# Kernel tuning notes

Hardware: AMD Instinct MI355X
Metric: run time of the kernel (lower is better)

The kernel has to match this reference:

```python
import jax, jax.numpy as jnp
import numpy as np

B, IN, H, OUT, L = 16384, 256, 256, 256, 7  # L = hidden_lstm_layer (cells beyond input cell)


def setup_inputs() -> dict:
    key = jax.random.key(0)
    ks = jax.random.split(key, 13)
    s = 0.05
    return {
        "x": jax.random.normal(ks[0], (B, IN), jnp.float32),
        "h_all": jax.random.normal(ks[1], (L + 1, B, H), jnp.float32),
        "c_all": jax.random.normal(ks[2], (L + 1, B, H), jnp.float32),
        # input LSTMCell params
        "Wih0": jax.random.normal(ks[3], (4 * H, IN), jnp.float32) * s,
        "Whh0": jax.random.normal(ks[4], (4 * H, H), jnp.float32) * s,
        "bih0": jax.random.normal(ks[5], (4 * H,), jnp.float32) * s,
        "bhh0": jax.random.normal(ks[6], (4 * H,), jnp.float32) * s,
        # stacked hidden LSTMCell params
        "Wih": jax.random.normal(ks[7], (L, 4 * H, H), jnp.float32) * s,
        "Whh": jax.random.normal(ks[8], (L, 4 * H, H), jnp.float32) * s,
        "bih": jax.random.normal(ks[9], (L, 4 * H), jnp.float32) * s,
        "bhh": jax.random.normal(ks[10], (L, 4 * H), jnp.float32) * s,
        # output Linear
        "Wout": jax.random.normal(ks[11], (OUT, H), jnp.float32) * s,
        "bout": jax.random.normal(ks[12], (OUT,), jnp.float32) * s,
    }


def _lstm_cell(x, h, c, Wi, Wh, bi, bh):
    # PyTorch LSTMCell: gates in (i, f, g, o) order along the 4H axis
    gates = x @ Wi.T + h @ Wh.T + (bi + bh)  # [B, 4H]
    i, f, g, o = jnp.split(gates, 4, axis=-1)
    c_new = jax.nn.sigmoid(f) * c + jax.nn.sigmoid(i) * jnp.tanh(g)
    h_new = jax.nn.sigmoid(o) * jnp.tanh(c_new)
    return h_new, c_new


def reference(x, h_all, c_all, Wih0, Whh0, bih0, bhh0, Wih, Whh, bih, bhh, Wout, bout):
    h, c = _lstm_cell(x, h_all[0], c_all[0], Wih0, Whh0, bih0, bhh0)
    hs, cs = [h], [c]
    for l in range(L):  # sequential layer-to-layer recurrence (structural)
        h, c = _lstm_cell(h, h_all[l + 1], c_all[l + 1], Wih[l], Whh[l], bih[l], bhh[l])
        hs.append(h)
        cs.append(c)
    output = h @ Wout.T + bout  # [B, OUT]
    return output, jnp.stack(hs), jnp.stack(cs)
```

## Files before the change

kernel.cpp:

```cpp
#include <hip/hip_runtime.h>
#include <stdint.h>

typedef __bf16 bf16;
typedef bf16 bf16x8 __attribute__((ext_vector_type(8)));
typedef bf16 bf16x4 __attribute__((ext_vector_type(4)));
typedef float f32x4 __attribute__((ext_vector_type(4)));

#define BROWS 16384
#define BM 128
#define BK 64
#define SL ((size_t)BROWS * 256)

__device__ __forceinline__ float sigmoidf_(float x) { return 1.0f / (1.0f + __expf(-x)); }
__device__ __forceinline__ float tanhf_(float x)    { return 1.0f - 2.0f / (1.0f + __expf(2.0f * x)); }

__device__ __forceinline__ bf16x4 cvt4(float4 v) {
    bf16x4 b; b[0] = (bf16)v.x; b[1] = (bf16)v.y; b[2] = (bf16)v.z; b[3] = (bf16)v.w;
    return b;
}

__device__ __forceinline__ void gload_lds16(const void* g, void* l) {
    __builtin_amdgcn_global_load_lds(
        (const __attribute__((address_space(1))) void*)g,
        (__attribute__((address_space(3))) void*)l, 16, 0, 0);
}


__global__ void convert_all(
    const float* __restrict__ s0, bf16* __restrict__ d0, unsigned n0,
    const float* __restrict__ s1, bf16* __restrict__ d1, unsigned n1,
    const float* __restrict__ s2, bf16* __restrict__ d2, unsigned n2,
    const float* __restrict__ s3, bf16* __restrict__ d3, unsigned n3,
    const float* __restrict__ s4, bf16* __restrict__ d4, unsigned n4,
    const float* __restrict__ s5, bf16* __restrict__ d5, unsigned n5,
    const float* __restrict__ s6, bf16* __restrict__ d6, unsigned n6)
{
    const unsigned total = n0 + n1 + n2 + n3 + n4 + n5 + n6;
    const unsigned stride = gridDim.x * blockDim.x;
    for (unsigned i = blockIdx.x * blockDim.x + threadIdx.x; i < total; i += stride) {
        unsigned idx = i;
        const float* src; bf16* dst;
        if      (idx < n0)         { src = s0; dst = d0; }
        else if ((idx -= n0) < n1) { src = s1; dst = d1; }
        else if ((idx -= n1) < n2) { src = s2; dst = d2; }
        else if ((idx -= n2) < n3) { src = s3; dst = d3; }
        else if ((idx -= n3) < n4) { src = s4; dst = d4; }
        else if ((idx -= n4) < n5) { src = s5; dst = d5; }
        else                       { idx -= n5; src = s6; dst = d6; }
        float4 v = *(const float4*)(src + (size_t)idx * 4);
        *(bf16x4*)(dst + (size_t)idx * 4) = cvt4(v);
    }
}

__global__ __launch_bounds__(256, 4) void lstm_cell_bf16(
    const bf16* __restrict__ A1, const bf16* __restrict__ A2,
    const bf16* __restrict__ W1, const bf16* __restrict__ W2,
    const float* __restrict__ b1, const float* __restrict__ b2,
    const float* __restrict__ Cin,
    float* __restrict__ Hout, float* __restrict__ Cout,
    bf16* __restrict__ Hb)
{
    __shared__ __align__(16) bf16 As[BM * BK];
    __shared__ __align__(16) bf16 Bs[BM * BK];

    const int tid  = threadIdx.x;
    const int lane = tid & 63;
    const int wave = tid >> 6;
    const int wm   = wave >> 1;
    const int wn   = wave & 1;
    const int quad = lane >> 4;
    const int l15  = lane & 15;
    const int row0 = blockIdx.x * BM;
    const int jblk = blockIdx.y * 32;

    const int srow  = lane >> 3;
    const int sslot = lane & 7;

    size_t aOff[4], bOff[4]; int ldsOff[4];
#pragma unroll
    for (int r4 = 0; r4 < 4; ++r4) {
        int rowT = r4 * 32 + wave * 8 + srow;
        int gsl  = (sslot ^ (rowT & 7)) * 8;
        aOff[r4] = (size_t)(row0 + rowT) * 256 + gsl;
        int gate = (rowT >> 4) & 3;
        int j    = jblk + (rowT & 15) + ((rowT >> 6) << 4);
        bOff[r4] = (size_t)(gate * 256 + j) * 256 + gsl;
        ldsOff[r4] = (r4 * 32 + wave * 8) * BK;
    }

    f32x4 acc[4][4];
#pragma unroll
    for (int i = 0; i < 4; ++i)
#pragma unroll
        for (int jj = 0; jj < 4; ++jj)
#pragma unroll
            for (int r = 0; r < 4; ++r) acc[i][jj][r] = 0.0f;

    for (int kIter = 0; kIter < 8; ++kIter) {
        const bf16* aSrc; const bf16* wSrc; int k0;
        if (kIter < 4) { aSrc = A1; wSrc = W1; k0 = kIter * BK; }
        else           { aSrc = A2; wSrc = W2; k0 = (kIter - 4) * BK; }

        __syncthreads();
#pragma unroll
        for (int r4 = 0; r4 < 4; ++r4)
            gload_lds16(aSrc + aOff[r4] + k0, &As[ldsOff[r4]]);
#pragma unroll
        for (int r4 = 0; r4 < 4; ++r4)
            gload_lds16(wSrc + bOff[r4] + k0, &Bs[ldsOff[r4]]);
        __syncthreads();

#pragma unroll
        for (int kk = 0; kk < BK; kk += 32) {
            const int sl0 = (kk >> 3) + quad;
            bf16x8 af[4], bfr[4];
#pragma unroll
            for (int mi = 0; mi < 4; ++mi) {
                int row = wm * 64 + mi * 16 + l15;
                int ps  = sl0 ^ (row & 7);
                af[mi] = *(const bf16x8*)&As[row * BK + ps * 8];
            }
#pragma unroll
            for (int ni = 0; ni < 4; ++ni) {
                int row = wn * 64 + ni * 16 + l15;
                int ps  = sl0 ^ (row & 7);
                bfr[ni] = *(const bf16x8*)&Bs[row * BK + ps * 8];
            }
#pragma unroll
            for (int mi = 0; mi < 4; ++mi)
#pragma unroll
                for (int ni = 0; ni < 4; ++ni)
                    acc[mi][ni] = __builtin_amdgcn_mfma_f32_16x16x32_bf16(
                        af[mi], bfr[ni], acc[mi][ni], 0, 0, 0);
        }
    }

    const int j = jblk + wn * 16 + l15;
    float bsum[4];
#pragma unroll
    for (int g = 0; g < 4; ++g)
        bsum[g] = b1[g * 256 + j] + b2[g * 256 + j];

#pragma unroll
    for (int mi = 0; mi < 4; ++mi) {
#pragma unroll
        for (int reg = 0; reg < 4; ++reg) {
            int row = row0 + wm * 64 + mi * 16 + quad * 4 + reg;
            float gi = acc[mi][0][reg] + bsum[0];
            float gf = acc[mi][1][reg] + bsum[1];
            float gg = acc[mi][2][reg] + bsum[2];
            float go = acc[mi][3][reg] + bsum[3];
            float c  = Cin[(size_t)row * 256 + j];
            float cn = sigmoidf_(gf) * c + sigmoidf_(gi) * tanhf_(gg);
            float hn = sigmoidf_(go) * tanhf_(cn);
            Hout[(size_t)row * 256 + j] = hn;
            Cout[(size_t)row * 256 + j] = cn;
            Hb[(size_t)row * 256 + j]   = (bf16)hn;
        }
    }
}

__global__ __launch_bounds__(256, 4) void linear_bf16(
    const bf16* __restrict__ A, const bf16* __restrict__ W,
    const float* __restrict__ bias, float* __restrict__ Out)
{
    __shared__ __align__(16) bf16 As[BM * BK];
    __shared__ __align__(16) bf16 Bs[BM * BK];

    const int tid  = threadIdx.x;
    const int lane = tid & 63;
    const int wave = tid >> 6;
    const int wm   = wave >> 1;
    const int wn   = wave & 1;
    const int quad = lane >> 4;
    const int l15  = lane & 15;
    const int row0 = blockIdx.x * BM;
    const int n0   = blockIdx.y * 128;

    const int srow  = lane >> 3;
    const int sslot = lane & 7;

    size_t aOff[4], bOff[4]; int ldsOff[4];
#pragma unroll
    for (int r4 = 0; r4 < 4; ++r4) {
        int rowT = r4 * 32 + wave * 8 + srow;
        int gsl  = (sslot ^ (rowT & 7)) * 8;
        aOff[r4] = (size_t)(row0 + rowT) * 256 + gsl;
        bOff[r4] = (size_t)(n0 + rowT) * 256 + gsl;
        ldsOff[r4] = (r4 * 32 + wave * 8) * BK;
    }

    f32x4 acc[4][4];
#pragma unroll
    for (int i = 0; i < 4; ++i)
#pragma unroll
        for (int jj = 0; jj < 4; ++jj)
#pragma unroll
            for (int r = 0; r < 4; ++r) acc[i][jj][r] = 0.0f;

    for (int kIter = 0; kIter < 4; ++kIter) {
        int k0 = kIter * BK;
        __syncthreads();
#pragma unroll
        for (int r4 = 0; r4 < 4; ++r4)
            gload_lds16(A + aOff[r4] + k0, &As[ldsOff[r4]]);
#pragma unroll
        for (int r4 = 0; r4 < 4; ++r4)
            gload_lds16(W + bOff[r4] + k0, &Bs[ldsOff[r4]]);
        __syncthreads();

#pragma unroll
        for (int kk = 0; kk < BK; kk += 32) {
            const int sl0 = (kk >> 3) + quad;
            bf16x8 af[4], bfr[4];
#pragma unroll
            for (int mi = 0; mi < 4; ++mi) {
                int row = wm * 64 + mi * 16 + l15;
                int ps  = sl0 ^ (row & 7);
                af[mi] = *(const bf16x8*)&As[row * BK + ps * 8];
            }
#pragma unroll
            for (int ni = 0; ni < 4; ++ni) {
                int row = wn * 64 + ni * 16 + l15;
                int ps  = sl0 ^ (row & 7);
                bfr[ni] = *(const bf16x8*)&Bs[row * BK + ps * 8];
            }
#pragma unroll
            for (int mi = 0; mi < 4; ++mi)
#pragma unroll
                for (int ni = 0; ni < 4; ++ni)
                    acc[mi][ni] = __builtin_amdgcn_mfma_f32_16x16x32_bf16(
                        af[mi], bfr[ni], acc[mi][ni], 0, 0, 0);
        }
    }

#pragma unroll
    for (int mi = 0; mi < 4; ++mi) {
#pragma unroll
        for (int ni = 0; ni < 4; ++ni) {
            int n = n0 + wn * 64 + ni * 16 + l15;
            float bv = bias[n];
#pragma unroll
            for (int reg = 0; reg < 4; ++reg) {
                int row = row0 + wm * 64 + mi * 16 + quad * 4 + reg;
                Out[(size_t)row * 256 + n] = acc[mi][ni][reg] + bv;
            }
        }
    }
}


__global__ __launch_bounds__(256, 2) void lstm_cell_kernel(
    const float* __restrict__ A1, const float* __restrict__ A2,
    const float* __restrict__ W1, const float* __restrict__ W2,
    const float* __restrict__ b1, const float* __restrict__ b2,
    const float* __restrict__ Cin,
    float* __restrict__ Hout, float* __restrict__ Cout)
{
    __shared__ __align__(16) bf16 As[BM * BK];
    __shared__ __align__(16) bf16 Bs[BM * BK];

    const int tid  = threadIdx.x;
    const int lane = tid & 63;
    const int wave = tid >> 6;
    const int wm   = wave >> 1;
    const int wn   = wave & 1;
    const int quad = lane >> 4;
    const int l15  = lane & 15;
    const int row0 = blockIdx.x * BM;
    const int jblk = blockIdx.y * 32;

    f32x4 acc[4][4];
#pragma unroll
    for (int i = 0; i < 4; ++i)
#pragma unroll
        for (int jj = 0; jj < 4; ++jj)
#pragma unroll
            for (int r = 0; r < 4; ++r) acc[i][jj][r] = 0.0f;

    for (int kIter = 0; kIter < 8; ++kIter) {
        const float* aSrc; const float* wSrc; int k0;
        if (kIter < 4) { aSrc = A1; wSrc = W1; k0 = kIter * BK; }
        else           { aSrc = A2; wSrc = W2; k0 = (kIter - 4) * BK; }

        __syncthreads();
#pragma unroll
        for (int it = 0; it < 8; ++it) {
            int c = it * 256 + tid;
            int r = c >> 4;
            int kc = c & 15;
            float4 va = *(const float4*)(aSrc + (size_t)(row0 + r) * 256 + k0 + kc * 4);
            *(bf16x4*)&As[r * BK + kc * 4] = cvt4(va);
            int gate = (r >> 4) & 3;
            int j    = jblk + (r & 15) + ((r >> 6) << 4);
            float4 vb = *(const float4*)(wSrc + (size_t)(gate * 256 + j) * 256 + k0 + kc * 4);
            *(bf16x4*)&Bs[r * BK + kc * 4] = cvt4(vb);
        }
        __syncthreads();

#pragma unroll
        for (int kk = 0; kk < BK; kk += 32) {
            bf16x8 af[4], bfr[4];
#pragma unroll
            for (int mi = 0; mi < 4; ++mi)
                af[mi] = *(const bf16x8*)&As[(wm * 64 + mi * 16 + l15) * BK + kk + quad * 8];
#pragma unroll
            for (int ni = 0; ni < 4; ++ni)
                bfr[ni] = *(const bf16x8*)&Bs[(wn * 64 + ni * 16 + l15) * BK + kk + quad * 8];
#pragma unroll
            for (int mi = 0; mi < 4; ++mi)
#pragma unroll
                for (int ni = 0; ni < 4; ++ni)
                    acc[mi][ni] = __builtin_amdgcn_mfma_f32_16x16x32_bf16(
                        af[mi], bfr[ni], acc[mi][ni], 0, 0, 0);
        }
    }

    const int j = jblk + wn * 16 + l15;
    float bsum[4];
#pragma unroll
    for (int g = 0; g < 4; ++g)
        bsum[g] = b1[g * 256 + j] + b2[g * 256 + j];

#pragma unroll
    for (int mi = 0; mi < 4; ++mi) {
#pragma unroll
        for (int reg = 0; reg < 4; ++reg) {
            int row = row0 + wm * 64 + mi * 16 + quad * 4 + reg;
            float gi = acc[mi][0][reg] + bsum[0];
            float gf = acc[mi][1][reg] + bsum[1];
            float gg = acc[mi][2][reg] + bsum[2];
            float go = acc[mi][3][reg] + bsum[3];
            float c  = Cin[(size_t)row * 256 + j];
            float cn = sigmoidf_(gf) * c + sigmoidf_(gi) * tanhf_(gg);
            float hn = sigmoidf_(go) * tanhf_(cn);
            Hout[(size_t)row * 256 + j] = hn;
            Cout[(size_t)row * 256 + j] = cn;
        }
    }
}

__global__ __launch_bounds__(256, 2) void linear_kernel(
    const float* __restrict__ A, const float* __restrict__ W,
    const float* __restrict__ bias, float* __restrict__ Out)
{
    __shared__ __align__(16) bf16 As[BM * BK];
    __shared__ __align__(16) bf16 Bs[BM * BK];

    const int tid  = threadIdx.x;
    const int lane = tid & 63;
    const int wave = tid >> 6;
    const int wm   = wave >> 1;
    const int wn   = wave & 1;
    const int quad = lane >> 4;
    const int l15  = lane & 15;
    const int row0 = blockIdx.x * BM;
    const int n0   = blockIdx.y * 128;

    f32x4 acc[4][4];
#pragma unroll
    for (int i = 0; i < 4; ++i)
#pragma unroll
        for (int jj = 0; jj < 4; ++jj)
#pragma unroll
            for (int r = 0; r < 4; ++r) acc[i][jj][r] = 0.0f;

    for (int kIter = 0; kIter < 4; ++kIter) {
        int k0 = kIter * BK;
        __syncthreads();
#pragma unroll
        for (int it = 0; it < 8; ++it) {
            int c = it * 256 + tid;
            int r = c >> 4, kc = c & 15;
            float4 va = *(const float4*)(A + (size_t)(row0 + r) * 256 + k0 + kc * 4);
            *(bf16x4*)&As[r * BK + kc * 4] = cvt4(va);
            float4 vb = *(const float4*)(W + (size_t)(n0 + r) * 256 + k0 + kc * 4);
            *(bf16x4*)&Bs[r * BK + kc * 4] = cvt4(vb);
        }
        __syncthreads();

#pragma unroll
        for (int kk = 0; kk < BK; kk += 32) {
            bf16x8 af[4], bfr[4];
#pragma unroll
            for (int mi = 0; mi < 4; ++mi)
                af[mi] = *(const bf16x8*)&As[(wm * 64 + mi * 16 + l15) * BK + kk + quad * 8];
#pragma unroll
            for (int ni = 0; ni < 4; ++ni)
                bfr[ni] = *(const bf16x8*)&Bs[(wn * 64 + ni * 16 + l15) * BK + kk + quad * 8];
#pragma unroll
            for (int mi = 0; mi < 4; ++mi)
#pragma unroll
                for (int ni = 0; ni < 4; ++ni)
                    acc[mi][ni] = __builtin_amdgcn_mfma_f32_16x16x32_bf16(
                        af[mi], bfr[ni], acc[mi][ni], 0, 0, 0);
        }
    }

#pragma unroll
    for (int mi = 0; mi < 4; ++mi) {
#pragma unroll
        for (int ni = 0; ni < 4; ++ni) {
            int n = n0 + wn * 64 + ni * 16 + l15;
            float bv = bias[n];
#pragma unroll
            for (int reg = 0; reg < 4; ++reg) {
                int row = row0 + wm * 64 + mi * 16 + quad * 4 + reg;
                Out[(size_t)row * 256 + n] = acc[mi][ni][reg] + bv;
            }
        }
    }
}

extern "C" void kernel_launch(void* const* d_in, const int* in_sizes, int n_in,
                              void* d_out, int out_size, void* d_ws, size_t ws_size,
                              hipStream_t stream) {
    const float* x     = (const float*)d_in[0];
    const float* h_all = (const float*)d_in[1];
    const float* c_all = (const float*)d_in[2];
    const float* Wih0  = (const float*)d_in[3];
    const float* Whh0  = (const float*)d_in[4];
    const float* bih0  = (const float*)d_in[5];
    const float* bhh0  = (const float*)d_in[6];
    const float* Wih   = (const float*)d_in[7];
    const float* Whh   = (const float*)d_in[8];
    const float* bih   = (const float*)d_in[9];
    const float* bhh   = (const float*)d_in[10];
    const float* Wout  = (const float*)d_in[11];
    const float* bout  = (const float*)d_in[12];
    float* out = (float*)d_out;

    float* hs = out + SL;
    float* cs = out + SL * 9;

    dim3 block(256);
    dim3 grid(BROWS / BM, 8);

    const size_t WS_NEEDED_BYTES = (size_t)50397184 * 2;

    if (d_ws != nullptr && ws_size >= WS_NEEDED_BYTES) {
        bf16* wsb   = (bf16*)d_ws;
        bf16* xb    = wsb;
        bf16* hball = xb    + 4194304;
        bf16* wih0b = hball + 33554432;
        bf16* whh0b = wih0b + 262144;
        bf16* wihb  = whh0b + 262144;
        bf16* whhb  = wihb  + 1835008;
        bf16* woutb = whhb  + 1835008;
        bf16* hbA   = woutb + 65536;
        bf16* hbB   = hbA   + 4194304;

        convert_all<<<2048, 256, 0, stream>>>(
            x,     xb,    4194304u  / 4,
            h_all, hball, 33554432u / 4,
            Wih0,  wih0b, 262144u   / 4,
            Whh0,  whh0b, 262144u   / 4,
            Wih,   wihb,  1835008u  / 4,
            Whh,   whhb,  1835008u  / 4,
            Wout,  woutb, 65536u    / 4);

        lstm_cell_bf16<<<grid, block, 0, stream>>>(
            xb, hball, wih0b, whh0b, bih0, bhh0, c_all, hs, cs, hbA);

        bf16* hprev = hbA; bf16* hcur = hbB;
        for (int l = 1; l <= 7; ++l) {
            lstm_cell_bf16<<<grid, block, 0, stream>>>(
                hprev,
                hball + (size_t)l * SL,
                wihb + (size_t)(l - 1) * 262144,
                whhb + (size_t)(l - 1) * 262144,
                bih + (size_t)(l - 1) * 1024,
                bhh + (size_t)(l - 1) * 1024,
                c_all + (size_t)l * SL,
                hs + (size_t)l * SL,
                cs + (size_t)l * SL,
                hcur);
            bf16* t = hprev; hprev = hcur; hcur = t;
        }

        linear_bf16<<<dim3(BROWS / BM, 2), block, 0, stream>>>(hprev, woutb, bout, out);
    } else {
        lstm_cell_kernel<<<grid, block, 0, stream>>>(
            x, h_all, Wih0, Whh0, bih0, bhh0, c_all, hs, cs);

        for (int l = 1; l <= 7; ++l) {
            lstm_cell_kernel<<<grid, block, 0, stream>>>(
                hs + (size_t)(l - 1) * SL,
                h_all + (size_t)l * SL,
                Wih + (size_t)(l - 1) * 1024 * 256,
                Whh + (size_t)(l - 1) * 1024 * 256,
                bih + (size_t)(l - 1) * 1024,
                bhh + (size_t)(l - 1) * 1024,
                c_all + (size_t)l * SL,
                hs + (size_t)l * SL,
                cs + (size_t)l * SL);
        }

        linear_kernel<<<dim3(BROWS / BM, 2), block, 0, stream>>>(
            hs + SL * 7, Wout, bout, out);
    }
}
```

Before: 743.7 us.

## Double-buffer LDS tiles in LSTM and linear GEMM kernels to overlap loads

Both GEMM kernels now keep two LDS buffers for the A and W tiles. Each iteration issues the async global-to-LDS copy for the next K tile before running the MFMAs on the current one, so only one barrier is needed per iteration instead of two. The goal is to hide global load latency behind matrix math. In exchange, LDS per block doubles to 64KB and launch bounds drop from 4 to 2 blocks per SM, which lowers the occupancy available for hiding latency.

New measurement: 741.6 us. No clear change (-0.3%).

```diff
diff --git a/kernel.cpp b/kernel.cpp
--- a/kernel.cpp
+++ b/kernel.cpp
@@ -52,7 +52,8 @@
     }
 }
 
-__global__ __launch_bounds__(256, 4) void lstm_cell_bf16(
+
+__global__ __launch_bounds__(256, 2) void lstm_cell_bf16(
     const bf16* __restrict__ A1, const bf16* __restrict__ A2,
     const bf16* __restrict__ W1, const bf16* __restrict__ W2,
     const float* __restrict__ b1, const float* __restrict__ b2,
@@ -60,8 +61,8 @@
     float* __restrict__ Hout, float* __restrict__ Cout,
     bf16* __restrict__ Hb)
 {
-    __shared__ __align__(16) bf16 As[BM * BK];
-    __shared__ __align__(16) bf16 Bs[BM * BK];
+    __shared__ __align__(16) bf16 As[2][BM * BK];
+    __shared__ __align__(16) bf16 Bs[2][BM * BK];
 
     const int tid  = threadIdx.x;
     const int lane = tid & 63;
@@ -96,20 +97,18 @@
 #pragma unroll
             for (int r = 0; r < 4; ++r) acc[i][jj][r] = 0.0f;
 
-    for (int kIter = 0; kIter < 8; ++kIter) {
+    auto STAGE = [&](int t, int buf) {
         const bf16* aSrc; const bf16* wSrc; int k0;
-        if (kIter < 4) { aSrc = A1; wSrc = W1; k0 = kIter * BK; }
-        else           { aSrc = A2; wSrc = W2; k0 = (kIter - 4) * BK; }
-
-        __syncthreads();
-#pragma unroll
-        for (int r4 = 0; r4 < 4; ++r4)
-            gload_lds16(aSrc + aOff[r4] + k0, &As[ldsOff[r4]]);
-#pragma unroll
-        for (int r4 = 0; r4 < 4; ++r4)
-            gload_lds16(wSrc + bOff[r4] + k0, &Bs[ldsOff[r4]]);
-        __syncthreads();
-
+        if (t < 4) { aSrc = A1; wSrc = W1; k0 = t * BK; }
+        else       { aSrc = A2; wSrc = W2; k0 = (t - 4) * BK; }
+#pragma unroll
+        for (int r4 = 0; r4 < 4; ++r4) {
+            gload_lds16(aSrc + aOff[r4] + k0, &As[buf][ldsOff[r4]]);
+            gload_lds16(wSrc + bOff[r4] + k0, &Bs[buf][ldsOff[r4]]);
+        }
+    };
+
+    auto COMPUTE = [&](int buf) {
 #pragma unroll
         for (int kk = 0; kk < BK; kk += 32) {
             const int sl0 = (kk >> 3) + quad;
@@ -118,13 +117,13 @@
             for (int mi = 0; mi < 4; ++mi) {
                 int row = wm * 64 + mi * 16 + l15;
                 int ps  = sl0 ^ (row & 7);
-                af[mi] = *(const bf16x8*)&As[row * BK + ps * 8];
+                af[mi] = *(const bf16x8*)&As[buf][row * BK + ps * 8];
             }
 #pragma unroll
             for (int ni = 0; ni < 4; ++ni) {
                 int row = wn * 64 + ni * 16 + l15;
                 int ps  = sl0 ^ (row & 7);
-                bfr[ni] = *(const bf16x8*)&Bs[row * BK + ps * 8];
+                bfr[ni] = *(const bf16x8*)&Bs[buf][row * BK + ps * 8];
             }
 #pragma unroll
             for (int mi = 0; mi < 4; ++mi)
@@ -133,6 +132,14 @@
                     acc[mi][ni] = __builtin_amdgcn_mfma_f32_16x16x32_bf16(
                         af[mi], bfr[ni], acc[mi][ni], 0, 0, 0);
         }
+    };
+
+    STAGE(0, 0);
+#pragma unroll
+    for (int t = 0; t < 8; ++t) {
+        __syncthreads();
+        if (t < 7) STAGE(t + 1, (t + 1) & 1);
+        COMPUTE(t & 1);
     }
 
     const int j = jblk + wn * 16 + l15;
@@ -160,12 +167,12 @@
     }
 }
 
-__global__ __launch_bounds__(256, 4) void linear_bf16(
+__global__ __launch_bounds__(256, 2) void linear_bf16(
     const bf16* __restrict__ A, const bf16* __restrict__ W,
     const float* __restrict__ bias, float* __restrict__ Out)
 {
-    __shared__ __align__(16) bf16 As[BM * BK];
-    __shared__ __align__(16) bf16 Bs[BM * BK];
+    __shared__ __align__(16) bf16 As[2][BM * BK];
+    __shared__ __align__(16) bf16 Bs[2][BM * BK];
 
     const int tid  = threadIdx.x;
     const int lane = tid & 63;
@@ -198,17 +205,16 @@
 #pragma unroll
             for (int r = 0; r < 4; ++r) acc[i][jj][r] = 0.0f;
 
-    for (int kIter = 0; kIter < 4; ++kIter) {
-        int k0 = kIter * BK;
-        __syncthreads();
-#pragma unroll
-        for (int r4 = 0; r4 < 4; ++r4)
-            gload_lds16(A + aOff[r4] + k0, &As[ldsOff[r4]]);
-#pragma unroll
-        for (int r4 = 0; r4 < 4; ++r4)
-            gload_lds16(W + bOff[r4] + k0, &Bs[ldsOff[r4]]);
-        __syncthreads();
-
+    auto STAGE = [&](int t, int buf) {
+        int k0 = t * BK;
+#pragma unroll
+        for (int r4 = 0; r4 < 4; ++r4) {
+            gload_lds16(A + aOff[r4] + k0, &As[buf][ldsOff[r4]]);
+            gload_lds16(W + bOff[r4] + k0, &Bs[buf][ldsOff[r4]]);
+        }
+    };
+
+    auto COMPUTE = [&](int buf) {
 #pragma unroll
         for (int kk = 0; kk < BK; kk += 32) {
             const int sl0 = (kk >> 3) + quad;
@@ -217,13 +223,13 @@
             for (int mi = 0; mi < 4; ++mi) {
                 int row = wm * 64 + mi * 16 + l15;
                 int ps  = sl0 ^ (row & 7);
-                af[mi] = *(const bf16x8*)&As[row * BK + ps * 8];
+                af[mi] = *(const bf16x8*)&As[buf][row * BK + ps * 8];
             }
 #pragma unroll
             for (int ni = 0; ni < 4; ++ni) {
                 int row = wn * 64 + ni * 16 + l15;
                 int ps  = sl0 ^ (row & 7);
-                bfr[ni] = *(const bf16x8*)&Bs[row * BK + ps * 8];
+                bfr[ni] = *(const bf16x8*)&Bs[buf][row * BK + ps * 8];
             }
 #pragma unroll
             for (int mi = 0; mi < 4; ++mi)
@@ -232,6 +238,14 @@
                     acc[mi][ni] = __builtin_amdgcn_mfma_f32_16x16x32_bf16(
                         af[mi], bfr[ni], acc[mi][ni], 0, 0, 0);
         }
+    };
+
+    STAGE(0, 0);
+#pragma unroll
+    for (int t = 0; t < 4; ++t) {
+        __syncthreads();
+        if (t < 3) STAGE(t + 1, (t + 1) & 1);
+        COMPUTE(t & 1);
     }
 
 #pragma unroll
```
